# Kernel optimization log

Hardware: AMD Instinct MI355X
Metric: run time of the kernel (lower is better)

## Reference

```python
import jax, jax.numpy as jnp
import numpy as np

N_NODES = 100000
N_EDGES = 1600000
NUM_FEATURES = 128
DIMS = [(NUM_FEATURES, 50), (50, 50), (50, 30), (30, 30), (30, 10), (10, 10), (10, 1)]


def setup_inputs() -> dict:
    key = jax.random.key(0)
    ks = jax.random.split(key, 4 + 2 * len(DIMS))
    inp = {
        "x": jax.random.normal(ks[0], (N_NODES, NUM_FEATURES), dtype=jnp.float32),
        "edge_index": jax.random.randint(ks[1], (2, N_EDGES), 0, N_NODES, dtype=jnp.int64) if jax.config.read("jax_enable_x64") else jax.random.randint(ks[1], (2, N_EDGES), 0, N_NODES, dtype=jnp.int32),
        "edge_weight": jax.random.uniform(ks[2], (N_EDGES,), dtype=jnp.float32),
    }
    for i, (fi, fo) in enumerate(DIMS):
        scale = 1.0 / np.sqrt(fi)
        inp[f"W{i+1}"] = jax.random.normal(ks[3 + 2 * i], (fi, fo), dtype=jnp.float32) * scale
        inp[f"b{i+1}"] = jax.random.normal(ks[4 + 2 * i], (fo,), dtype=jnp.float32) * 0.01
    return inp


def _gcn_norm(edge_index, edge_weight, n):
    # Add self-loops with weight 1, then symmetric normalization (PyG GCNConv).
    loops = jnp.arange(n)
    row = jnp.concatenate([edge_index[0], loops])
    col = jnp.concatenate([edge_index[1], loops])
    w = jnp.concatenate([edge_weight, jnp.ones((n,), edge_weight.dtype)])
    deg = jnp.zeros((n,), edge_weight.dtype).at[col].add(w)
    dinv = jnp.where(deg > 0, 1.0 / jnp.sqrt(deg), 0.0)
    norm = dinv[row] * w * dinv[col]
    return row, col, norm


def _gcn_conv(x, row, col, norm, W, b):
    h = x @ W                                # [N, out]
    msg = h[row] * norm[:, None]             # gather + edge scale [E+N, out]
    out = jnp.zeros_like(h).at[col].add(msg) # scatter-add
    return out + b


def _forward(x, edge_index, edge_weight, params):
    n = x.shape[0]
    row, col, norm = _gcn_norm(edge_index, edge_weight, n)  # shared across layers
    h = x
    n_layers = len(params)
    for i, (W, b) in enumerate(params):
        h = _gcn_conv(h, row, col, norm, W, b)
        if i < n_layers - 1:
            h = jax.nn.relu(h)
        # F.dropout treated as identity (eval mode) for a deterministic reference
    return h


def reference(x, edge_index, edge_weight, W1, b1, W2, b2, W3, b3, W4, b4, W5, b5, W6, b6, W7, b7):
    params = [(W1, b1), (W2, b2), (W3, b3), (W4, b4), (W5, b5), (W6, b6), (W7, b7)]
    return _forward(x, edge_index, edge_weight, params)
```

## Files before the change

### kernel.cpp

```cpp
#include <hip/hip_runtime.h>
#include <hip/hip_fp16.h>


static constexpr int NN = 100000;
static constexpr int NE = 1600000;
static constexpr int BKL = 9;
static constexpr int NBUK = (NN + 511) >> BKL;
static constexpr int EPT = 8;
static constexpr int EB = (NE + 2047) / 2048;


__global__ __launch_bounds__(256) void k_hist0(const int* __restrict__ col,
                                               int* __restrict__ counts) {
    __shared__ int lh[NBUK];
    for (int j = threadIdx.x; j < NBUK; j += 256) lh[j] = 0;
    __syncthreads();
    int base = blockIdx.x * 2048;
#pragma unroll
    for (int k = 0; k < EPT; ++k) {
        int e = base + k * 256 + threadIdx.x;
        if (e < NE) atomicAdd(&lh[col[e] >> BKL], 1);
    }
    __syncthreads();
    for (int j = threadIdx.x; j < NBUK; j += 256)
        counts[j * EB + blockIdx.x] = lh[j];
}


__global__ __launch_bounds__(256) void k_scanA(int* __restrict__ counts,
                                               int* __restrict__ btot) {
    __shared__ int lds[256];
    const int b = blockIdx.x;
    const int t = threadIdx.x;
    int* c = counts + (size_t)b * EB;
    constexpr int PER = (EB + 255) / 256;
    int v[PER];
    int s = 0;
#pragma unroll
    for (int k = 0; k < PER; ++k) {
        int idx = t * PER + k;
        v[k] = (idx < EB) ? c[idx] : 0;
        s += v[k];
    }
    lds[t] = s;
    __syncthreads();
    for (int off = 1; off < 256; off <<= 1) {
        int u = (t >= off) ? lds[t - off] : 0;
        __syncthreads();
        lds[t] += u;
        __syncthreads();
    }
    int run = lds[t] - s;
#pragma unroll
    for (int k = 0; k < PER; ++k) {
        int idx = t * PER + k;
        if (idx < EB) { c[idx] = run; run += v[k]; }
    }
    if (t == 255) btot[b] = lds[255];
}


__global__ void k_scanB(const int* __restrict__ btot, int* __restrict__ bstart) {
    __shared__ int lds[256];
    int t = threadIdx.x;
    int v = (t < NBUK) ? btot[t] : 0;
    lds[t] = v;
    __syncthreads();
    for (int off = 1; off < 256; off <<= 1) {
        int u = (t >= off) ? lds[t - off] : 0;
        __syncthreads();
        lds[t] += u;
        __syncthreads();
    }
    if (t < NBUK) bstart[t] = lds[t] - v;
    if (t == 0) bstart[NBUK] = NE;
}


__global__ __launch_bounds__(256) void k_A1(const int* __restrict__ row,
                                            const int* __restrict__ col,
                                            const float* __restrict__ ew,
                                            const int* __restrict__ counts,
                                            const int* __restrict__ bstart,
                                            int2* __restrict__ stg) {
    __shared__ int cur[NBUK];
    for (int j = threadIdx.x; j < NBUK; j += 256)
        cur[j] = bstart[j] + counts[j * EB + blockIdx.x];
    __syncthreads();
    int base = blockIdx.x * 2048;
#pragma unroll
    for (int k = 0; k < EPT; ++k) {
        int e = base + k * 256 + threadIdx.x;
        if (e < NE) {
            int c = col[e], r = row[e];
            int pos = atomicAdd(&cur[c >> BKL], 1);
            stg[pos] = make_int2(((c & 511) << 17) | r, __float_as_int(ew[e]));
        }
    }
}


__global__ __launch_bounds__(256) void k_bdeg(const int* __restrict__ bstart,
                                              const int2* __restrict__ stg,
                                              float* __restrict__ dinv) {
    __shared__ float sdeg[512];
    const int b = blockIdx.x;
    for (int j = threadIdx.x; j < 512; j += 256) sdeg[j] = 0.0f;
    __syncthreads();
    const int s = bstart[b], e = bstart[b + 1];
    for (int p = s + threadIdx.x; p < e; p += 256) {
        int2 rec = stg[p];
        atomicAdd(&sdeg[rec.x >> 17], __int_as_float(rec.y));
    }
    __syncthreads();
    for (int j = threadIdx.x; j < 512; j += 256) {
        int idx = (b << BKL) + j;
        if (idx < NN) dinv[idx] = rsqrtf(sdeg[j] + 1.0f);
    }
}


__global__ __launch_bounds__(512) void k_place(const int* __restrict__ bstart,
                                               const int2* __restrict__ stg,
                                               const float* __restrict__ dinv,
                                               int* __restrict__ offs,
                                               int2* __restrict__ csw) {
    __shared__ int lcnt[512];
    __shared__ int cur[512];
    const int b = blockIdx.x;
    const int t = threadIdx.x;
    lcnt[t] = 0;
    __syncthreads();
    const int s = bstart[b], e = bstart[b + 1];
    for (int p = s + t; p < e; p += 512)
        atomicAdd(&lcnt[stg[p].x >> 17], 1);
    __syncthreads();
    int v = lcnt[t];
    for (int off = 1; off < 512; off <<= 1) {
        int u = (t >= off) ? lcnt[t - off] : 0;
        __syncthreads();
        lcnt[t] += u;
        __syncthreads();
    }
    int excl = lcnt[t] - v;
    int idx = (b << BKL) + t;
    if (idx <= NN) offs[idx] = s + excl;
    cur[t] = s + excl;
    __syncthreads();
    for (int p = s + t; p < e; p += 512) {
        int2 rec = stg[p];
        int cl = rec.x >> 17;
        int r = rec.x & 0x1FFFF;
        float nw = dinv[r] * __int_as_float(rec.y) * dinv[(b << BKL) + cl];
        int slot = atomicAdd(&cur[cl], 1);
        csw[slot] = make_int2(r, __float_as_int(nw));
    }
}


typedef short s16x8 __attribute__((ext_vector_type(8)));
typedef float f32x4v __attribute__((ext_vector_type(4)));
typedef _Float16 f16x8 __attribute__((ext_vector_type(8)));

static __device__ __forceinline__ unsigned short bf16rn(float f) {
    unsigned u = __float_as_uint(f);
    return (unsigned short)((u + 0x7FFFu + ((u >> 16) & 1u)) >> 16);
}

static constexpr int WT2 = 16384;
static constexpr int WT3 = WT2 + 9216;
static constexpr int WT4 = WT3 + 4608;
static constexpr int WT5 = WT4 + 2560;
static constexpr int WT_TOT = WT5 + 1280;

static __device__ __forceinline__ void prep_f16(const float* __restrict__ W,
                                                int FIN, int FOUT, int KP,
                                                int PITCH, int NCT,
                                                short* __restrict__ dst, int t) {
    const int WCNT = NCT * 16 * PITCH;
    for (int li = t; li < NCT * 16 * KP; li += 256) {
        const int c = li / KP, k = li - c * KP;
        float f = (c < FOUT && k < FIN) ? W[k * FOUT + c] : 0.f;
        __half hh = __float2half_rn(f);
        __half hl = __float2half_rn(f - __half2float(hh));
        dst[c * PITCH + k] = __half_as_short(hh);
        dst[WCNT + c * PITCH + k] = __half_as_short(hl);
    }
}

__global__ void k_wprep(const float* __restrict__ W0, const float* __restrict__ W1,
                        const float* __restrict__ W2, const float* __restrict__ W3,
                        const float* __restrict__ W4, short* __restrict__ wt) {
    const int t = threadIdx.x;
    const int blk = blockIdx.x;
    if (blk < 2) {
#pragma unroll
        for (int i = 0; i < 16; ++i) {
            const int li = t + 256 * (16 * blk + i);
            const int c = li >> 7, k = li & 127;
            float f = (c < 50) ? W0[k * 50 + c] : 0.f;
            unsigned short hb = bf16rn(f);
            float hf = __uint_as_float((unsigned)hb << 16);
            unsigned short lb = bf16rn(f - hf);
            const int off = c * 128 + (k ^ ((c & 7) << 3));
            wt[off] = (short)hb;
            wt[8192 + off] = (short)lb;
        }
    } else if (blk == 2) prep_f16(W1, 50, 50, 64, 72, 4, wt + WT2, t);
    else if (blk == 3)   prep_f16(W2, 50, 30, 64, 72, 2, wt + WT3, t);
    else if (blk == 4)   prep_f16(W3, 30, 30, 32, 40, 2, wt + WT4, t);
    else                 prep_f16(W4, 30, 10, 32, 40, 1, wt + WT5, t);
}


__global__ __launch_bounds__(256, 4) void k_matmul_f(const float* __restrict__ X,
                                                     const short* __restrict__ wt,
                                                     __half* __restrict__ H) {
    __shared__ short lds[2 * 64 * 128];
    const int t = threadIdx.x;
    {
        const int4* src = (const int4*)wt;
        int4* dst = (int4*)lds;
#pragma unroll
        for (int j = 0; j < 8; ++j) dst[j * 256 + t] = src[j * 256 + t];
    }
    const int w = t >> 6;
    const int lane = t & 63;
    const int lr = lane & 15;
    const int kg = lane >> 4;
    const int row = blockIdx.x * 64 + 16 * w + lr;
    const float* xr = X + (size_t)(row < NN ? row : NN - 1) * 128 + kg * 8;

    float4 xa[4][2];
#pragma unroll
    for (int kb = 0; kb < 4; ++kb) {
        xa[kb][0] = *(const float4*)(xr + kb * 32);
        xa[kb][1] = *(const float4*)(xr + kb * 32 + 4);
    }
    __syncthreads();

    f32x4v acc[4];
#pragma unroll
    for (int ct = 0; ct < 4; ++ct) acc[ct] = (f32x4v){0.f, 0.f, 0.f, 0.f};

#pragma unroll
    for (int kb = 0; kb < 4; ++kb) {
        s16x8 ah, al;
        const unsigned* xu = (const unsigned*)&xa[kb][0];
#pragma unroll
        for (int e = 0; e < 8; ++e) {
            const unsigned u = xu[e];
            const float lo = __uint_as_float(u) - __uint_as_float(u & 0xFFFF0000u);
            ah[e] = (short)(u >> 16);
            al[e] = (short)(__float_as_uint(lo) >> 16);
        }
        const int kf = kb * 32 + kg * 8;
        s16x8 bh[4], bl[4];
#pragma unroll
        for (int ct = 0; ct < 4; ++ct) {
            const int bc = ct * 16 + lr;
            const int ko = bc * 128 + (kf ^ ((bc & 7) << 3));
            bh[ct] = *(const s16x8*)&lds[ko];
            bl[ct] = *(const s16x8*)&lds[8192 + ko];
        }
#pragma unroll
        for (int ct = 0; ct < 4; ++ct)
            acc[ct] = __builtin_amdgcn_mfma_f32_16x16x32_bf16(ah, bh[ct], acc[ct], 0, 0, 0);
#pragma unroll
        for (int ct = 0; ct < 4; ++ct)
            acc[ct] = __builtin_amdgcn_mfma_f32_16x16x32_bf16(ah, bl[ct], acc[ct], 0, 0, 0);
#pragma unroll
        for (int ct = 0; ct < 4; ++ct)
            acc[ct] = __builtin_amdgcn_mfma_f32_16x16x32_bf16(al, bh[ct], acc[ct], 0, 0, 0);
    }

    const int gr = blockIdx.x * 64 + 16 * w + kg * 4;
#pragma unroll
    for (int ct = 0; ct < 4; ++ct) {
        const int col = ct * 16 + lr;
        if (col < 50) {
#pragma unroll
            for (int rg = 0; rg < 4; ++rg) {
                const int orow = gr + rg;
                if (orow < NN)
                    H[(size_t)orow * 64 + col] = __float2half_rn(acc[ct][rg]);
            }
        }
    }
}


template <int FIN, int KP, int PITCH, int SX, int FOUT, int NCT, int S>
__global__ __launch_bounds__(256, 4) void k_matmul_fh(const __half* __restrict__ X,
                                                      const short* __restrict__ wt,
                                                      __half* __restrict__ H) {
    constexpr int NKB = KP / 32;
    constexpr int WCNT = NCT * 16 * PITCH;
    __shared__ short lds[2 * WCNT];
    const int t = threadIdx.x;
    {
        const int4* src = (const int4*)wt;
        int4* dst = (int4*)lds;
        constexpr int NI = (2 * WCNT) / 8;
        for (int j = t; j < NI; j += 256) dst[j] = src[j];
    }
    const int w = t >> 6;
    const int lane = t & 63;
    const int lr = lane & 15;
    const int kg = lane >> 4;
    const int row = blockIdx.x * 64 + 16 * w + lr;
    const __half* xr = X + (size_t)(row < NN ? row : NN - 1) * SX + kg * 8;

    int4 xa[NKB];
#pragma unroll
    for (int kb = 0; kb < NKB; ++kb) xa[kb] = *(const int4*)(xr + kb * 32);
    __syncthreads();

    f32x4v acc[NCT];
#pragma unroll
    for (int ct = 0; ct < NCT; ++ct) acc[ct] = (f32x4v){0.f, 0.f, 0.f, 0.f};

#pragma unroll
    for (int kb = 0; kb < NKB; ++kb) {
        f16x8 a = *(const f16x8*)&xa[kb];
        const int kf = kb * 32 + kg * 8;
#pragma unroll
        for (int ct = 0; ct < NCT; ++ct) {
            const int c = ct * 16 + lr;
            f16x8 bh = *(const f16x8*)&lds[c * PITCH + kf];
            f16x8 bl = *(const f16x8*)&lds[WCNT + c * PITCH + kf];
            acc[ct] = __builtin_amdgcn_mfma_f32_16x16x32_f16(a, bh, acc[ct], 0, 0, 0);
            acc[ct] = __builtin_amdgcn_mfma_f32_16x16x32_f16(a, bl, acc[ct], 0, 0, 0);
        }
    }

    const int gr = blockIdx.x * 64 + 16 * w + kg * 4;
#pragma unroll
    for (int ct = 0; ct < NCT; ++ct) {
        const int col = ct * 16 + lr;
        if (col < FOUT) {
#pragma unroll
            for (int rg = 0; rg < 4; ++rg) {
                const int orow = gr + rg;
                if (orow < NN)
                    H[(size_t)orow * S + col] = __float2half_rn(acc[ct][rg]);
            }
        }
    }
}


template <int FIN, int SX, int FOUT, int S, int NSPL>
__global__ __launch_bounds__(256, 2) void k_matmul_h(const __half* __restrict__ X,
                                                     const float* __restrict__ W,
                                                     __half* __restrict__ H) {
    constexpr int FC = FOUT / NSPL;
    constexpr int NCH = (FIN + 7) / 8;
    const int node = blockIdx.x * 256 + threadIdx.x;
    const int ch = blockIdx.y;
    if (node >= NN) return;
    const __half* xr = X + (size_t)node * SX;
    int4 raw[NCH];
#pragma unroll
    for (int c = 0; c < NCH; ++c) raw[c] = *(const int4*)(xr + 8 * c);
    float acc[FC];
#pragma unroll
    for (int j = 0; j < FC; ++j) acc[j] = 0.0f;
#pragma unroll
    for (int c = 0; c < NCH; ++c) {
        const __half2* hp = (const __half2*)&raw[c];
        const int lim = (FIN - 8 * c < 8) ? FIN - 8 * c : 8;
#pragma unroll
        for (int kk = 0; kk < 8; ++kk) {
            if (kk < lim) {
                __half2 pair = hp[kk >> 1];
                float xv = (kk & 1) ? __high2float(pair) : __low2float(pair);
                const float* wrow = W + (8 * c + kk) * FOUT + ch * FC;
#pragma unroll
                for (int j = 0; j < FC; ++j) acc[j] = fmaf(xv, wrow[j], acc[j]);
            }
        }
    }
    __half* hr = H + (size_t)node * S + ch * FC;
#pragma unroll
    for (int j = 0; j < FC; ++j) hr[j] = __float2half_rn(acc[j]);
}

__global__ void k_matmul_1h(const __half* __restrict__ X, const float* __restrict__ W,
                            float* __restrict__ H) {
    int i = blockIdx.x * blockDim.x + threadIdx.x;
    if (i >= NN) return;
    const __half* xr = X + (size_t)i * 16;
    int4 r0 = *(const int4*)xr;
    __half2 r1 = *(const __half2*)(xr + 8);
    const __half2* hp = (const __half2*)&r0;
    float acc = 0.0f;
#pragma unroll
    for (int q = 0; q < 4; ++q) {
        acc = fmaf(__low2float(hp[q]), W[2 * q], acc);
        acc = fmaf(__high2float(hp[q]), W[2 * q + 1], acc);
    }
    acc = fmaf(__low2float(r1), W[8], acc);
    acc = fmaf(__high2float(r1), W[9], acc);
    H[i] = acc;
}


static __device__ __forceinline__ int2 nt_load2(const int2* p) {
    unsigned long long raw = __builtin_nontemporal_load((const unsigned long long*)p);
    return make_int2((int)(raw & 0xFFFFFFFFull), (int)(raw >> 32));
}

template <int F, int SH, int SA, int LPN, bool RELU>
__global__ __launch_bounds__(256) void k_agg2(const int* __restrict__ offs,
                                              const int2* __restrict__ csw,
                                              const __half2* __restrict__ H,
                                              const float* __restrict__ dinv,
                                              const float* __restrict__ b,
                                              __half* __restrict__ O) {
    constexpr int R = F / 2;
    int t = blockIdx.x * blockDim.x + threadIdx.x;
    int g = t / LPN;
    int f = t - g * LPN;
    if (g >= NN) return;
    const int q0 = 4 * f;
    __half2* orow = (__half2*)(O + (size_t)g * SA) + q0;
    if (q0 >= R) {
        const __half2 z = __floats2half2_rn(0.f, 0.f);
#pragma unroll
        for (int c = 0; c < 4; ++c)
            if (q0 + c < SA / 2) orow[c] = z;
        return;
    }
    int p = offs[g];
    const int pe = offs[g + 1];
    const int pl = pe - 1;

    float2 acc[4];
#pragma unroll
    for (int c = 0; c < 4; ++c) acc[c] = make_float2(0.f, 0.f);

    for (; p < pe; p += 8) {
        int2 e[8];
#pragma unroll
        for (int i = 0; i < 8; ++i) e[i] = nt_load2(csw + min(p + i, pl));
        __half2 h[8][4];
#pragma unroll
        for (int i = 0; i < 8; ++i)
            *(int4*)h[i] = *(const int4*)(H + (size_t)e[i].x * SH + q0);
#pragma unroll
        for (int i = 0; i < 8; ++i) {
            float w = (p + i < pe) ? __int_as_float(e[i].y) : 0.0f;
#pragma unroll
            for (int c = 0; c < 4; ++c) {
                acc[c].x = fmaf(__low2float(h[i][c]), w, acc[c].x);
                acc[c].y = fmaf(__high2float(h[i][c]), w, acc[c].y);
            }
        }
    }

    float di = dinv[g];
    float d2 = di * di;
    __half2 hs[4];
    *(int4*)hs = *(const int4*)(H + (size_t)g * SH + q0);
#pragma unroll
    for (int c = 0; c < 4; ++c) {
        if (q0 + c < R) {
            float vx = acc[c].x + fmaf(__low2float(hs[c]), d2, b[2 * (q0 + c)]);
            float vy = acc[c].y + fmaf(__high2float(hs[c]), d2, b[2 * (q0 + c) + 1]);
            if (RELU) { vx = fmaxf(vx, 0.f); vy = fmaxf(vy, 0.f); }
            orow[c] = __floats2half2_rn(vx, vy);
        } else if (q0 + c < SA / 2) {
            orow[c] = __floats2half2_rn(0.f, 0.f);
        }
    }
}

__global__ void k_agg1(const int* __restrict__ offs, const int2* __restrict__ csw,
                       const float* __restrict__ H, const float* __restrict__ dinv,
                       const float* __restrict__ b, float* __restrict__ O) {
    int g = blockIdx.x * blockDim.x + threadIdx.x;
    if (g >= NN) return;
    int p = offs[g];
    const int pe = offs[g + 1];
    const int pl = pe - 1;
    float a[8];
#pragma unroll
    for (int i = 0; i < 8; ++i) a[i] = 0.f;
    for (; p < pe; p += 8) {
        int2 e[8];
#pragma unroll
        for (int i = 0; i < 8; ++i) e[i] = nt_load2(csw + min(p + i, pl));
        float hv[8];
#pragma unroll
        for (int i = 0; i < 8; ++i) hv[i] = H[e[i].x];
#pragma unroll
        for (int i = 0; i < 8; ++i) {
            float w = (p + i < pe) ? __int_as_float(e[i].y) : 0.f;
            a[i] = fmaf(hv[i], w, a[i]);
        }
    }
    float di = dinv[g];
    float s = ((a[0] + a[1]) + (a[2] + a[3])) + ((a[4] + a[5]) + (a[6] + a[7]));
    O[g] = s + fmaf(H[g], di * di, b[0]);
}


static inline size_t alignup(size_t x) { return (x + 255) & ~(size_t)255; }

extern "C" void kernel_launch(void* const* d_in, const int* in_sizes, int n_in,
                              void* d_out, int out_size, void* d_ws, size_t ws_size,
                              hipStream_t stream) {
    const float* x  = (const float*)d_in[0];
    const int*   ei = (const int*)d_in[1];
    const float* ew = (const float*)d_in[2];
    const float* Wp[7];
    const float* Bp[7];
    for (int l = 0; l < 7; ++l) {
        Wp[l] = (const float*)d_in[3 + 2 * l];
        Bp[l] = (const float*)d_in[4 + 2 * l];
    }
    const int* row = ei;
    const int* col = ei + NE;

    char* ws = (char*)d_ws;
    float* dinv  = (float*)ws;  ws += alignup((size_t)NN * 4);
    char*  Hb    = ws;          ws += alignup((size_t)NN * 64 * 2);
    char*  Aa    = ws;          ws += alignup((size_t)NN * 64 * 2);
    char*  Ab    = ws;          ws += alignup((size_t)NN * 64 * 2);
    int*   offs  = (int*)ws;    ws += alignup((size_t)(NN + 1) * 4);
    int*   counts= (int*)ws;    ws += alignup((size_t)NBUK * EB * 4);
    int*   btot  = (int*)ws;    ws += alignup((size_t)NBUK * 4);
    int*   bstart= (int*)ws;    ws += alignup((size_t)(NBUK + 1) * 4);
    int2*  stg   = (int2*)ws;   ws += alignup((size_t)NE * 8);
    int2*  csw   = (int2*)ws;   ws += alignup((size_t)NE * 8);
    short* wt    = (short*)ws;  ws += alignup((size_t)WT_TOT * 2);

    const int gN = (NN + 255) / 256;
    const int gM = (NN + 63) / 64;

    k_wprep<<<6, 256, 0, stream>>>(Wp[0], Wp[1], Wp[2], Wp[3], Wp[4], wt);
    k_hist0<<<EB, 256, 0, stream>>>(col, counts);
    k_scanA<<<NBUK, 256, 0, stream>>>(counts, btot);
    k_scanB<<<1, 256, 0, stream>>>(btot, bstart);
    k_A1<<<EB, 256, 0, stream>>>(row, col, ew, counts, bstart, stg);
    k_bdeg<<<NBUK, 256, 0, stream>>>(bstart, stg, dinv);
    k_place<<<NBUK, 512, 0, stream>>>(bstart, stg, dinv, offs, csw);

#define AGG(FOUT, S, LPN, RELU, OUT, LIDX)                                                  \
    k_agg2<FOUT, (S) / 2, S, LPN, RELU>                                                     \
        <<<((size_t)NN * (LPN) + 255) / 256, 256, 0, stream>>>(                             \
            offs, csw, (const __half2*)Hb, dinv, Bp[LIDX], (__half*)(OUT))

    k_matmul_f<<<gM, 256, 0, stream>>>(x, wt, (__half*)Hb);
    AGG(50, 64, 8, true, Aa, 0);
    k_matmul_fh<50, 64, 72, 64, 50, 4, 64><<<gM, 256, 0, stream>>>((const __half*)Aa, wt + WT2, (__half*)Hb);
    AGG(50, 64, 8, true, Ab, 1);
    k_matmul_fh<50, 64, 72, 64, 30, 2, 32><<<gM, 256, 0, stream>>>((const __half*)Ab, wt + WT3, (__half*)Hb);
    AGG(30, 32, 4, true, Aa, 2);
    k_matmul_fh<30, 32, 40, 32, 30, 2, 32><<<gM, 256, 0, stream>>>((const __half*)Aa, wt + WT4, (__half*)Hb);
    AGG(30, 32, 4, true, Ab, 3);
    k_matmul_fh<30, 32, 40, 32, 10, 1, 16><<<gM, 256, 0, stream>>>((const __half*)Ab, wt + WT5, (__half*)Hb);
    AGG(10, 16, 2, true, Aa, 4);
    k_matmul_h<10, 16, 10, 16, 1><<<dim3(gN, 1), 256, 0, stream>>>((const __half*)Aa, Wp[5], (__half*)Hb);
    AGG(10, 16, 2, true, Ab, 5);
#undef AGG

    k_matmul_1h<<<gN, 256, 0, stream>>>((const __half*)Ab, Wp[6], (float*)Hb);
    k_agg1<<<gN, 256, 0, stream>>>(offs, csw, (const float*)Hb, dinv, Bp[6],
                                   (float*)d_out);
}
```

Baseline: 418.4 us.

## Sort nodes by in-degree to balance aggregation wavefront workloads

Adds a counting sort of nodes by in-degree (histogram, two-level scan, placement) producing a permutation. The aggregation kernels process nodes in permuted order, so lanes in a wavefront have similar edge counts, cutting divergence from uneven degrees. In exchange there are four extra small kernel launches, and the row/output accesses become scattered through the permutation, which hurts coalescing of the H self-term and output writes.

```diff
diff --git a/kernel.cpp b/kernel.cpp
--- a/kernel.cpp
+++ b/kernel.cpp
@@ -8,6 +8,7 @@
 static constexpr int NBUK = (NN + 511) >> BKL;
 static constexpr int EPT = 8;
 static constexpr int EB = (NE + 2047) / 2048;
+static constexpr int SNB = (NN + 255) / 256;
 
 
 __global__ __launch_bounds__(256) void k_hist0(const int* __restrict__ col,
@@ -154,6 +155,85 @@
         float nw = dinv[r] * __int_as_float(rec.y) * dinv[(b << BKL) + cl];
         int slot = atomicAdd(&cur[cl], 1);
         csw[slot] = make_int2(r, __float_as_int(nw));
+    }
+}
+
+
+__global__ __launch_bounds__(256) void k_shist(const int* __restrict__ offs,
+                                               int* __restrict__ scnt) {
+    __shared__ int lh[64];
+    const int t = threadIdx.x;
+    if (t < 64) lh[t] = 0;
+    __syncthreads();
+    const int g = blockIdx.x * 256 + t;
+    if (g < NN) {
+        int d = offs[g + 1] - offs[g];
+        atomicAdd(&lh[min(d, 63)], 1);
+    }
+    __syncthreads();
+    if (t < 64) scnt[t * SNB + blockIdx.x] = lh[t];
+}
+
+__global__ __launch_bounds__(256) void k_sscanA(int* __restrict__ scnt,
+                                                int* __restrict__ stot) {
+    __shared__ int lds[256];
+    const int b = blockIdx.x;
+    const int t = threadIdx.x;
+    int* c = scnt + (size_t)b * SNB;
+    constexpr int PER = (SNB + 255) / 256;
+    int v[PER];
+    int s = 0;
+#pragma unroll
+    for (int k = 0; k < PER; ++k) {
+        int idx = t * PER + k;
+        v[k] = (idx < SNB) ? c[idx] : 0;
+        s += v[k];
+    }
+    lds[t] = s;
+    __syncthreads();
+    for (int off = 1; off < 256; off <<= 1) {
+        int u = (t >= off) ? lds[t - off] : 0;
+        __syncthreads();
+        lds[t] += u;
+        __syncthreads();
+    }
+    int run = lds[t] - s;
+#pragma unroll
+    for (int k = 0; k < PER; ++k) {
+        int idx = t * PER + k;
+        if (idx < SNB) { c[idx] = run; run += v[k]; }
+    }
+    if (t == 255) stot[b] = lds[255];
+}
+
+__global__ void k_sscanB(const int* __restrict__ stot, int* __restrict__ sbst) {
+    __shared__ int lds[64];
+    int t = threadIdx.x;
+    int v = stot[t];
+    lds[t] = v;
+    __syncthreads();
+    for (int off = 1; off < 64; off <<= 1) {
+        int u = (t >= off) ? lds[t - off] : 0;
+        __syncthreads();
+        lds[t] += u;
+        __syncthreads();
+    }
+    sbst[t] = lds[t] - v;
+}
+
+__global__ __launch_bounds__(256) void k_splace(const int* __restrict__ offs,
+                                                const int* __restrict__ scnt,
+                                                const int* __restrict__ sbst,
+                                                int* __restrict__ perm) {
+    __shared__ int cur[64];
+    const int t = threadIdx.x;
+    if (t < 64) cur[t] = sbst[t] + scnt[t * SNB + blockIdx.x];
+    __syncthreads();
+    const int g = blockIdx.x * 256 + t;
+    if (g < NN) {
+        int d = offs[g + 1] - offs[g];
+        int pos = atomicAdd(&cur[min(d, 63)], 1);
+        perm[pos] = g;
     }
 }
 
@@ -413,6 +493,7 @@
 
 template <int F, int SH, int SA, int LPN, bool RELU>
 __global__ __launch_bounds__(256) void k_agg2(const int* __restrict__ offs,
+                                              const int* __restrict__ perm,
                                               const int2* __restrict__ csw,
                                               const __half2* __restrict__ H,
                                               const float* __restrict__ dinv,
@@ -420,9 +501,10 @@
                                               __half* __restrict__ O) {
     constexpr int R = F / 2;
     int t = blockIdx.x * blockDim.x + threadIdx.x;
-    int g = t / LPN;
-    int f = t - g * LPN;
-    if (g >= NN) return;
+    int gidx = t / LPN;
+    int f = t - gidx * LPN;
+    if (gidx >= NN) return;
+    const int g = perm[gidx];
     const int q0 = 4 * f;
     __half2* orow = (__half2*)(O + (size_t)g * SA) + q0;
     if (q0 >= R) {
@@ -476,11 +558,13 @@
     }
 }
 
-__global__ void k_agg1(const int* __restrict__ offs, const int2* __restrict__ csw,
+__global__ void k_agg1(const int* __restrict__ offs, const int* __restrict__ perm,
+                       const int2* __restrict__ csw,
                        const float* __restrict__ H, const float* __restrict__ dinv,
                        const float* __restrict__ b, float* __restrict__ O) {
-    int g = blockIdx.x * blockDim.x + threadIdx.x;
-    if (g >= NN) return;
+    int gi = blockIdx.x * blockDim.x + threadIdx.x;
+    if (gi >= NN) return;
+    const int g = perm[gi];
     int p = offs[g];
     const int pe = offs[g + 1];
     const int pl = pe - 1;
@@ -535,6 +619,10 @@
     int2*  stg   = (int2*)ws;   ws += alignup((size_t)NE * 8);
     int2*  csw   = (int2*)ws;   ws += alignup((size_t)NE * 8);
     short* wt    = (short*)ws;  ws += alignup((size_t)WT_TOT * 2);
+    int*   scnt  = (int*)ws;    ws += alignup((size_t)64 * SNB * 4);
+    int*   stot  = (int*)ws;    ws += alignup((size_t)64 * 4);
+    int*   sbst  = (int*)ws;    ws += alignup((size_t)64 * 4);
+    int*   perm  = (int*)ws;    ws += alignup((size_t)NN * 4);
 
     const int gN = (NN + 255) / 256;
     const int gM = (NN + 63) / 64;
@@ -546,11 +634,15 @@
     k_A1<<<EB, 256, 0, stream>>>(row, col, ew, counts, bstart, stg);
     k_bdeg<<<NBUK, 256, 0, stream>>>(bstart, stg, dinv);
     k_place<<<NBUK, 512, 0, stream>>>(bstart, stg, dinv, offs, csw);
+    k_shist<<<SNB, 256, 0, stream>>>(offs, scnt);
+    k_sscanA<<<64, 256, 0, stream>>>(scnt, stot);
+    k_sscanB<<<1, 64, 0, stream>>>(stot, sbst);
+    k_splace<<<SNB, 256, 0, stream>>>(offs, scnt, sbst, perm);
 
 #define AGG(FOUT, S, LPN, RELU, OUT, LIDX)                                                  \
     k_agg2<FOUT, (S) / 2, S, LPN, RELU>                                                     \
         <<<((size_t)NN * (LPN) + 255) / 256, 256, 0, stream>>>(                             \
-            offs, csw, (const __half2*)Hb, dinv, Bp[LIDX], (__half*)(OUT))
+            offs, perm, csw, (const __half2*)Hb, dinv, Bp[LIDX], (__half*)(OUT))
 
     k_matmul_f<<<gM, 256, 0, stream>>>(x, wt, (__half*)Hb);
     AGG(50, 64, 8, true, Aa, 0);
@@ -567,6 +659,6 @@
 #undef AGG
 
     k_matmul_1h<<<gN, 256, 0, stream>>>((const __half*)Ab, Wp[6], (float*)Hb);
-    k_agg1<<<gN, 256, 0, stream>>>(offs, csw, (const float*)Hb, dinv, Bp[6],
+    k_agg1<<<gN, 256, 0, stream>>>(offs, perm, csw, (const float*)Hb, dinv, Bp[6],
                                    (float*)d_out);
 }
```

New measurement: 444.7 us. 6.3% more time.
